# Kernel tuning notes

Hardware: AMD Instinct MI355X
Metric: run time of the kernel (lower is better)

Reference implementation:

```python
import jax, jax.numpy as jnp
import numpy as np

N_QUBITS = 6
N_SHARED_LAYERS = 3
N_TASK_LAYERS = 2
ENC_HIDDEN = 256
INPUT_DIM = 784
BATCH = 256
P1Q = 0.001  # 1-qubit depolarizing prob
P2Q = 0.01   # 2-qubit-gate depolarizing approximation (applied as 1q channel, as in source)

C = jnp.complex64
PX = jnp.array([[0, 1], [1, 0]], C)
PY = jnp.array([[0, -1j], [1j, 0]], C)
PZ = jnp.array([[1, 0], [0, -1]], C)
CNOT = jnp.array([[1, 0, 0, 0], [0, 1, 0, 0], [0, 0, 0, 1], [0, 0, 1, 0]], C)

_LOW = 'abcdefghijklmnopqrstuvwxyz'


def _apply(dm, G, axes, batched):
    # contract gate G (rows=out, cols=in) into dm along absolute dm axes `axes`
    k = len(axes)
    G = G.reshape(G.shape[:G.ndim - 2] + (2,) * (2 * k))
    nd = dm.ndim - 1  # 2 * n_qubits
    dm_sub = ['Z'] + list(_LOW[:nd])
    out_sub = list(dm_sub)
    new = 'ABCD'
    gout, gin = [], []
    for j, ax in enumerate(axes):
        gout.append(new[j]); gin.append(dm_sub[ax]); out_sub[ax] = new[j]
    g_str = ('Z' if batched else '') + ''.join(gout) + ''.join(gin)
    return jnp.einsum(f"{g_str},{''.join(dm_sub)}->{''.join(out_sub)}", G, dm)


def apply_unitary(dm, U, wires, n, batched=False):
    # rho -> U rho U^dagger; ket axes are 1+w, bra axes 1+n+w
    dm = _apply(dm, U, [1 + w for w in wires], batched)
    return _apply(dm, jnp.conj(U), [1 + n + w for w in wires], batched)


def depolarize(dm, p, q, n):
    x = apply_unitary(dm, PX, [q], n)
    y = apply_unitary(dm, PY, [q], n)
    z = apply_unitary(dm, PZ, [q], n)
    return (1.0 - p) * dm + (p / 3.0) * (x + y + z)


def rot_mat(phi, theta, omega):
    # PennyLane Rot(phi, theta, omega) = RZ(omega) RY(theta) RZ(phi)
    c = jnp.cos(theta / 2)
    s = jnp.sin(theta / 2)
    ep = jnp.exp(-0.5j * (phi + omega))  # e^{-i(phi+omega)/2}
    em = jnp.exp(0.5j * (phi - omega))   # e^{+i(phi-omega)/2}
    return jnp.stack([jnp.stack([ep * c, -em * s]),
                      jnp.stack([jnp.conj(em) * s, jnp.conj(ep) * c])]).astype(C)


def ry_batched(theta):
    # theta: (B,) -> (B,2,2)
    c = jnp.cos(theta / 2)
    s = jnp.sin(theta / 2)
    return jnp.stack([jnp.stack([c, -s], -1),
                      jnp.stack([s, c], -1)], -2).astype(C)


def strongly_entangling(dm, w, n):
    # PennyLane StronglyEntanglingLayers, default ranges r = (l % (n-1)) + 1, CNOT ring
    L = w.shape[0]
    for l in range(L):
        for i in range(n):
            dm = apply_unitary(dm, rot_mat(w[l, i, 0], w[l, i, 1], w[l, i, 2]), [i], n)
        r = (l % (n - 1)) + 1
        for i in range(n):
            dm = apply_unitary(dm, CNOT, [i, (i + r) % n], n)
    return dm


def circuit(z, shared_w, task_w):
    n = N_QUBITS
    Bz = z.shape[0]
    dm = jnp.zeros((Bz,) + (2,) * (2 * n), C).at[(slice(None),) + (0,) * (2 * n)].set(1.0)
    for i in range(n):
        dm = apply_unitary(dm, ry_batched(z[:, i] * jnp.pi), [i], n, batched=True)
        dm = depolarize(dm, P1Q, i, n)
    dm = strongly_entangling(dm, shared_w, n)
    for i in range(n):
        dm = depolarize(dm, P1Q, i, n)
    for i in range(n - 1):
        dm = depolarize(dm, P2Q, i, n)
    dm = strongly_entangling(dm, task_w, n)
    for i in range(n):
        dm = depolarize(dm, P1Q, i, n)
    D = 2 ** n
    probs = jnp.real(jnp.diagonal(dm.reshape(Bz, D, D), axis1=1, axis2=2))  # (B, D)
    bits = (jnp.arange(D)[:, None] >> jnp.arange(n - 1, -1, -1)[None, :]) & 1  # wire 0 = MSB
    signs = (1 - 2 * bits).astype(jnp.float32)  # (D, n)
    return probs.astype(jnp.float32) @ signs    # (B, n) = <Z_i>


def setup_inputs():
    key = jax.random.key(0)
    ks = jax.random.split(key, 8)
    f = jnp.float32
    return {
        "x": jax.random.normal(ks[0], (BATCH, INPUT_DIM), f),
        "W1": jax.random.normal(ks[1], (ENC_HIDDEN, INPUT_DIM), f) * 0.03,
        "b1": jnp.zeros((ENC_HIDDEN,), f),
        "ln_g": jnp.ones((ENC_HIDDEN,), f),
        "ln_b": jnp.zeros((ENC_HIDDEN,), f),
        "W2": jax.random.normal(ks[2], (N_QUBITS, ENC_HIDDEN), f) * 0.05,
        "b2": jnp.zeros((N_QUBITS,), f),
        "shared_w": jax.random.normal(ks[3], (N_SHARED_LAYERS, N_QUBITS, 3), f) * 0.1,
        "task_w": jax.random.normal(ks[4], (N_TASK_LAYERS, N_QUBITS, 3), f) * 0.1,
        "Wp": jax.random.normal(ks[5], (2, N_QUBITS), f) * 0.1,
        "bp": jnp.zeros((2,), f),
    }


def reference(x, W1, b1, ln_g, ln_b, W2, b2, shared_w, task_w, Wp, bp):
    # encoder: Linear -> ReLU -> LayerNorm -> Linear -> Tanh
    h = jnp.maximum(x @ W1.T + b1, 0.0)
    mu = h.mean(-1, keepdims=True)
    var = ((h - mu) ** 2).mean(-1, keepdims=True)
    h = (h - mu) / jnp.sqrt(var + 1e-5) * ln_g + ln_b
    z = jnp.tanh(h @ W2.T + b2)            # (B, N_QUBITS)
    ev = circuit(z, shared_w, task_w)      # (B, N_QUBITS)
    return ev @ Wp.T + bp                  # (B, 2)
```

## Files before the change

### kernel.cpp

```cpp
#include <hip/hip_runtime.h>
#include <math.h>

#define NQ 6
#define BLK 1024
#define HID 256
#define INDIM 784

#define PW1 0.001f
#define PW2 0.01f
constexpr float WO1 = 1.f - 4.f * PW1 / 3.f;
constexpr float WO2 = 1.f - 4.f * PW2 / 3.f;
constexpr float WOc = WO1 * WO2;

struct alignas(16) RingTabs { int t[3][4096]; };
constexpr RingTabs make_ring_tabs() {
    RingTabs R{};
    for (int ri = 0; ri < 3; ++ri) {
        int r = ri + 1;
        for (int v = 0; v < 4096; ++v) {
            int x[6], z[6];
            for (int w = 0; w < 6; ++w) { x[w] = (v >> (2 * w + 1)) & 1; z[w] = (v >> (2 * w)) & 1; }
            int sgn = 0;
            for (int i = 5; i >= 0; --i) {
                int c = i, tg = (i + r) % 6;
                sgn ^= x[c] & z[tg] & (x[tg] ^ z[c] ^ 1);
                x[tg] ^= x[c];
                z[c]  ^= z[tg];
            }
            int s = 0;
            for (int w = 0; w < 6; ++w) s |= (x[w] << (2 * w + 1)) | (z[w] << (2 * w));
            R.t[ri][v] = s | (sgn << 31);
        }
    }
    return R;
}
static __device__ const RingTabs RT = make_ring_tabs();

__device__ __forceinline__ int swz(int n) {
    return n ^ ((((n >> 6) ^ (n >> 10)) & 3) << 3);
}

template<int CTRL>
__device__ __forceinline__ float qb(float v) {
    int r = __builtin_amdgcn_update_dpp(0, __builtin_bit_cast(int, v), CTRL, 0xF, 0xF, true);
    return __builtin_bit_cast(float, r);
}
template<int OFF>
__device__ __forceinline__ float swzl(float v) {
    return __builtin_bit_cast(float, __builtin_amdgcn_ds_swizzle(__builtin_bit_cast(int, v), OFF));
}

__device__ __forceinline__ void rot_reg(float e[4], float4 rZ, float4 rX, float4 rY) {
    float X = e[2], Y = e[3], Z = e[1];
    e[2] = fmaf(rX.x, X, fmaf(rX.y, Y, rX.z * Z));
    e[3] = fmaf(rY.x, X, fmaf(rY.y, Y, rY.z * Z));
    e[1] = fmaf(rZ.x, X, fmaf(rZ.y, Y, rZ.z * Z));
}
__device__ __forceinline__ void rot_q1(float e[4], float4 cf) {
    #pragma unroll
    for (int j = 0; j < 4; ++j) {
        float vZ = qb<0x55>(e[j]);
        float vX = qb<0xAA>(e[j]);
        float vY = qb<0xFF>(e[j]);
        e[j] = fmaf(cf.x, vX, fmaf(cf.y, vY, fmaf(cf.z, vZ, cf.w * e[j])));
    }
}
__device__ __forceinline__ void rot_q2(float e[4], float4 cf) {
    #pragma unroll
    for (int j = 0; j < 4; ++j) {
        float vZ = swzl<0x093>(e[j]);
        float vX = swzl<0x113>(e[j]);
        float vY = swzl<0x193>(e[j]);
        e[j] = fmaf(cf.x, vX, fmaf(cf.y, vY, fmaf(cf.z, vZ, cf.w * e[j])));
    }
}
__device__ __forceinline__ void rot_q3(float e[4], float4 cf, int lane) {
    int s1 = (lane & 15) | 16, s2 = (lane & 15) | 32, s3 = (lane & 15) | 48;
    #pragma unroll
    for (int j = 0; j < 4; ++j) {
        float vZ = __shfl(e[j], s1, 64);
        float vX = __shfl(e[j], s2, 64);
        float vY = __shfl(e[j], s3, 64);
        e[j] = fmaf(cf.x, vX, fmaf(cf.y, vY, fmaf(cf.z, vZ, cf.w * e[j])));
    }
}


__global__ __launch_bounds__(BLK)
void nqm_kernel(const float* __restrict__ x, const float* __restrict__ W1,
                const float* __restrict__ b1, const float* __restrict__ ln_g,
                const float* __restrict__ ln_b, const float* __restrict__ W2,
                const float* __restrict__ b2, const float* __restrict__ shared_w,
                const float* __restrict__ task_w, const float* __restrict__ Wp,
                const float* __restrict__ bp, float* __restrict__ out)
{
    __shared__ __align__(16) float dmA[4096];
    __shared__ __align__(16) float dmB[4096];
    __shared__ float4 xrow[INDIM / 4];
    __shared__ float hpart[1024];
    __shared__ __align__(16) float4 Mlane[30][4];
    __shared__ float bloch[NQ][4];
    __shared__ float red[4], red2[4];
    __shared__ float zpart[4][8];
    __shared__ float bcast[2];
    __shared__ float evs[8];

    const int tid = threadIdx.x;
    const int b = blockIdx.x;
    const int wv = tid >> 6;
    const int lane = tid & 63;

    if (tid < INDIM / 4) xrow[tid] = ((const float4*)(x + (size_t)b * INDIM))[tid];
    __syncthreads();

    {
        const int u = tid & 255, p = tid >> 8;
        const float4* w1v = (const float4*)(W1 + (size_t)u * INDIM) + p * 49;
        const float4* xv4 = xrow + p * 49;
        float acc = 0.0f;
        #pragma unroll 7
        for (int k = 0; k < 49; ++k) {
            float4 wvv = w1v[k];
            float4 xv = xv4[k];
            acc = fmaf(wvv.x, xv.x, acc);
            acc = fmaf(wvv.y, xv.y, acc);
            acc = fmaf(wvv.z, xv.z, acc);
            acc = fmaf(wvv.w, xv.w, acc);
        }
        hpart[p * 256 + u] = acc;
    }
    __syncthreads();

    float h = 0.0f;
    if (tid < 256) {
        h = hpart[tid] + hpart[256 + tid] + hpart[512 + tid] + hpart[768 + tid] + b1[tid];
        h = fmaxf(h, 0.0f);
        float s = h, s2 = h * h;
        #pragma unroll
        for (int off = 32; off > 0; off >>= 1) {
            s  += __shfl_down(s, off, 64);
            s2 += __shfl_down(s2, off, 64);
        }
        if (lane == 0) { red[tid >> 6] = s; red2[tid >> 6] = s2; }
    }
    __syncthreads();
    if (tid == 0) {
        float ts  = red[0] + red[1] + red[2] + red[3];
        float ts2 = red2[0] + red2[1] + red2[2] + red2[3];
        float mu  = ts * (1.0f / HID);
        float var = ts2 * (1.0f / HID) - mu * mu;
        bcast[0] = mu;
        bcast[1] = rsqrtf(var + 1e-5f);
    }
    __syncthreads();
    if (tid < 256) {
        float hnj = (h - bcast[0]) * bcast[1] * ln_g[tid] + ln_b[tid];
        float p[NQ];
        #pragma unroll
        for (int i = 0; i < NQ; ++i) p[i] = hnj * W2[i * HID + tid];
        #pragma unroll
        for (int off = 32; off > 0; off >>= 1) {
            #pragma unroll
            for (int i = 0; i < NQ; ++i) p[i] += __shfl_down(p[i], off, 64);
        }
        if (lane == 0) {
            #pragma unroll
            for (int i = 0; i < NQ; ++i) zpart[tid >> 6][i] = p[i];
        }
    }
    __syncthreads();

    if (tid < NQ) {
        float z = zpart[0][tid] + zpart[1][tid] + zpart[2][tid] + zpart[3][tid] + b2[tid];
        z = tanhf(z);
        float sn, c;
        sincosf(z * 3.14159265358979323846f, &sn, &c);
        bloch[tid][0] = 1.0f;
        bloch[tid][1] = WO1 * c;
        bloch[tid][2] = WO1 * sn;
        bloch[tid][3] = 0.0f;
    } else if (tid < 36) {
        int g = tid - NQ;
        int layer = g / NQ;
        int wire = g % NQ;
        const float* w = (layer < 3) ? (shared_w + (layer * NQ + wire) * 3)
                                     : (task_w + ((layer - 3) * NQ + wire) * 3);
        float phi = w[0], theta = w[1], omega = w[2];
        float sf, cf_, st, ct, so, co;
        sincosf(phi, &sf, &cf_);
        sincosf(theta, &st, &ct);
        sincosf(omega, &so, &co);
        float M00 = co * ct * cf_ - so * sf;
        float M01 = -co * ct * sf - so * cf_;
        float M02 = co * st;
        float M10 = so * ct * cf_ + co * sf;
        float M11 = -so * ct * sf + co * cf_;
        float M12 = so * st;
        float M20 = -st * cf_;
        float M21 = st * sf;
        float M22 = ct;
        float f = (layer == 3) ? ((wire < 5) ? WOc : WO1) : 1.0f;
        Mlane[g][0] = make_float4(0.f, 0.f, 0.f, 1.f);
        Mlane[g][1] = make_float4(f * M20, f * M21, f * M22, 0.f);
        Mlane[g][2] = make_float4(f * M00, f * M01, f * M02, 0.f);
        Mlane[g][3] = make_float4(f * M10, f * M11, f * M12, 0.f);
    }

    const int q1 = lane & 3, q2 = (lane >> 2) & 3, q3 = (lane >> 4) & 3;
    const int q4 = wv & 3, q5 = wv >> 2;
    const int baseB = ((lane & 3) << 10) | (wv << 4) | (lane >> 2);
    const int rtab[4] = {0, 1, 2, 0};
    __syncthreads();

    for (int l = 0; l < 5; ++l) {
        const int g0 = l * 6;
        float e[4];

        if (l == 0) {
            float A = bloch[1][q1] * bloch[2][q2] * bloch[3][q3] * bloch[4][q4] * bloch[5][q5];
            e[0] = A * bloch[0][0];
            e[1] = A * bloch[0][1];
            e[2] = A * bloch[0][2];
            e[3] = A * bloch[0][3];
        } else {
            const int4 te = *(const int4*)&RT.t[rtab[l - 1]][tid << 2];
            float v0 = dmA[swz(te.x & 4095)];
            float v1 = dmA[swz(te.y & 4095)];
            float v2 = dmA[swz(te.z & 4095)];
            float v3 = dmA[swz(te.w & 4095)];
            e[0] = __int_as_float(__float_as_int(v0) ^ (te.x & 0x80000000));
            e[1] = __int_as_float(__float_as_int(v1) ^ (te.y & 0x80000000));
            e[2] = __int_as_float(__float_as_int(v2) ^ (te.z & 0x80000000));
            e[3] = __int_as_float(__float_as_int(v3) ^ (te.w & 0x80000000));
        }
        rot_reg(e, Mlane[g0 + 0][1], Mlane[g0 + 0][2], Mlane[g0 + 0][3]);
        rot_q1(e, Mlane[g0 + 1][q1]);
        rot_q2(e, Mlane[g0 + 2][q2]);
        rot_q3(e, Mlane[g0 + 3][q3], lane);
        *(float4*)&dmB[swz(tid << 2)] = make_float4(e[0], e[1], e[2], e[3]);
        __syncthreads();

        e[0] = dmB[swz(baseB)];
        e[1] = dmB[swz(baseB + 256)];
        e[2] = dmB[swz(baseB + 512)];
        e[3] = dmB[swz(baseB + 768)];
        rot_reg(e, Mlane[g0 + 4][1], Mlane[g0 + 4][2], Mlane[g0 + 4][3]);
        rot_q1(e, Mlane[g0 + 5][lane & 3]);
        dmA[swz(baseB)]       = e[0];
        dmA[swz(baseB + 256)] = e[1];
        dmA[swz(baseB + 512)] = e[2];
        dmA[swz(baseB + 768)] = e[3];
        __syncthreads();
    }

    if (tid < NQ) {
        int e = RT.t[1][1 << (2 * tid)];
        float v = dmA[swz(e & 4095)];
        v = __int_as_float(__float_as_int(v) ^ (e & 0x80000000));
        evs[tid] = WO1 * v;
    }
    __syncthreads();
    if (tid < 2) {
        float o = bp[tid];
        #pragma unroll
        for (int i = 0; i < NQ; ++i) o = fmaf(evs[i], Wp[tid * NQ + i], o);
        out[b * 2 + tid] = o;
    }
}

extern "C" void kernel_launch(void* const* d_in, const int* in_sizes, int n_in,
                              void* d_out, int out_size, void* d_ws, size_t ws_size,
                              hipStream_t stream) {
    (void)in_sizes; (void)n_in; (void)d_ws; (void)ws_size; (void)out_size;
    const float* x        = (const float*)d_in[0];
    const float* W1       = (const float*)d_in[1];
    const float* b1       = (const float*)d_in[2];
    const float* ln_g     = (const float*)d_in[3];
    const float* ln_b     = (const float*)d_in[4];
    const float* W2       = (const float*)d_in[5];
    const float* b2       = (const float*)d_in[6];
    const float* shared_w = (const float*)d_in[7];
    const float* task_w   = (const float*)d_in[8];
    const float* Wp       = (const float*)d_in[9];
    const float* bp       = (const float*)d_in[10];
    float* out = (float*)d_out;

    hipLaunchKernelGGL(nqm_kernel, dim3(256), dim3(BLK), 0, stream,
                       x, W1, b1, ln_g, ln_b, W2, b2, shared_w, task_w, Wp, bp, out);
}
```

Baseline: 103.2 us.

## Split encoder GEMM into separate tiled split-K kernel writing partials to workspace

Moves the x·W1ᵀ encoder matmul out of the fused per-sample kernel into its own kernel. That kernel uses 32x32 output tiles with split-K over 4 slices, staged through shared memory. The old code had every block stream the whole 784x256 W1 matrix for a single row; the new tiling reuses W1 across 32 batch rows. The cost is a second kernel launch plus a write and re-read of partial sums through global workspace.

```diff
diff --git a/kernel.cpp b/kernel.cpp
--- a/kernel.cpp
+++ b/kernel.cpp
@@ -85,19 +85,60 @@
     }
 }
 
+__global__ __launch_bounds__(256)
+void enc_gemm(const float* __restrict__ x, const float* __restrict__ W1,
+              float* __restrict__ hp)
+{
+    __shared__ float xsT[196][32];
+    __shared__ float wsT[196][32];
+    const int tid = threadIdx.x;
+    const int bid = blockIdx.x;
+    const int tile = bid >> 2, s = bid & 3;
+    const int bb = (tile >> 3) * 32, bu = (tile & 7) * 32;
+    const int k0 = s * 196;
+
+    for (int i = tid; i < 3136; i += 256) {
+        int r = i & 31;
+        int cb = i >> 5;
+        int m = (cb >= 49);
+        int c = cb - m * 49;
+        const float* src = m ? (W1 + (size_t)(bu + r) * INDIM + k0 + 4 * c)
+                             : (x  + (size_t)(bb + r) * INDIM + k0 + 4 * c);
+        float4 v = *(const float4*)src;
+        float (*dst)[32] = m ? wsT : xsT;
+        dst[4 * c + 0][r] = v.x;
+        dst[4 * c + 1][r] = v.y;
+        dst[4 * c + 2][r] = v.z;
+        dst[4 * c + 3][r] = v.w;
+    }
+    __syncthreads();
+
+    const int tx = tid & 15, ty = tid >> 4;
+    float a00 = 0.f, a01 = 0.f, a10 = 0.f, a11 = 0.f;
+    #pragma unroll 4
+    for (int k = 0; k < 196; ++k) {
+        float2 xv = *(const float2*)&xsT[k][2 * ty];
+        float2 wv = *(const float2*)&wsT[k][2 * tx];
+        a00 = fmaf(xv.x, wv.x, a00);
+        a01 = fmaf(xv.x, wv.y, a01);
+        a10 = fmaf(xv.y, wv.x, a10);
+        a11 = fmaf(xv.y, wv.y, a11);
+    }
+    float* o = hp + (size_t)s * 65536 + (size_t)(bb + 2 * ty) * 256 + bu + 2 * tx;
+    o[0] = a00; o[1] = a01;
+    o[256] = a10; o[257] = a11;
+}
 
 __global__ __launch_bounds__(BLK)
-void nqm_kernel(const float* __restrict__ x, const float* __restrict__ W1,
-                const float* __restrict__ b1, const float* __restrict__ ln_g,
-                const float* __restrict__ ln_b, const float* __restrict__ W2,
-                const float* __restrict__ b2, const float* __restrict__ shared_w,
-                const float* __restrict__ task_w, const float* __restrict__ Wp,
-                const float* __restrict__ bp, float* __restrict__ out)
+void nqm_kernel(const float* __restrict__ hp, const float* __restrict__ b1,
+                const float* __restrict__ ln_g, const float* __restrict__ ln_b,
+                const float* __restrict__ W2, const float* __restrict__ b2,
+                const float* __restrict__ shared_w, const float* __restrict__ task_w,
+                const float* __restrict__ Wp, const float* __restrict__ bp,
+                float* __restrict__ out)
 {
     __shared__ __align__(16) float dmA[4096];
     __shared__ __align__(16) float dmB[4096];
-    __shared__ float4 xrow[INDIM / 4];
-    __shared__ float hpart[1024];
     __shared__ __align__(16) float4 Mlane[30][4];
     __shared__ float bloch[NQ][4];
     __shared__ float red[4], red2[4];
@@ -110,30 +151,10 @@
     const int wv = tid >> 6;
     const int lane = tid & 63;
 
-    if (tid < INDIM / 4) xrow[tid] = ((const float4*)(x + (size_t)b * INDIM))[tid];
-    __syncthreads();
-
-    {
-        const int u = tid & 255, p = tid >> 8;
-        const float4* w1v = (const float4*)(W1 + (size_t)u * INDIM) + p * 49;
-        const float4* xv4 = xrow + p * 49;
-        float acc = 0.0f;
-        #pragma unroll 7
-        for (int k = 0; k < 49; ++k) {
-            float4 wvv = w1v[k];
-            float4 xv = xv4[k];
-            acc = fmaf(wvv.x, xv.x, acc);
-            acc = fmaf(wvv.y, xv.y, acc);
-            acc = fmaf(wvv.z, xv.z, acc);
-            acc = fmaf(wvv.w, xv.w, acc);
-        }
-        hpart[p * 256 + u] = acc;
-    }
-    __syncthreads();
-
     float h = 0.0f;
     if (tid < 256) {
-        h = hpart[tid] + hpart[256 + tid] + hpart[512 + tid] + hpart[768 + tid] + b1[tid];
+        const float* hb = hp + (size_t)b * 256 + tid;
+        h = hb[0] + hb[65536] + hb[131072] + hb[196608] + b1[tid];
         h = fmaxf(h, 0.0f);
         float s = h, s2 = h * h;
         #pragma unroll
@@ -271,7 +292,7 @@
 extern "C" void kernel_launch(void* const* d_in, const int* in_sizes, int n_in,
                               void* d_out, int out_size, void* d_ws, size_t ws_size,
                               hipStream_t stream) {
-    (void)in_sizes; (void)n_in; (void)d_ws; (void)ws_size; (void)out_size;
+    (void)in_sizes; (void)n_in; (void)ws_size; (void)out_size;
     const float* x        = (const float*)d_in[0];
     const float* W1       = (const float*)d_in[1];
     const float* b1       = (const float*)d_in[2];
@@ -284,7 +305,9 @@
     const float* Wp       = (const float*)d_in[9];
     const float* bp       = (const float*)d_in[10];
     float* out = (float*)d_out;
-
+    float* hp  = (float*)d_ws;
+
+    hipLaunchKernelGGL(enc_gemm, dim3(256), dim3(256), 0, stream, x, W1, hp);
     hipLaunchKernelGGL(nqm_kernel, dim3(256), dim3(BLK), 0, stream,
-                       x, W1, b1, ln_g, ln_b, W2, b2, shared_w, task_w, Wp, bp, out);
-}
+                       hp, b1, ln_g, ln_b, W2, b2, shared_w, task_w, Wp, bp, out);
+}
```

Measured after the change: 95.53 us. 1.08x faster.
